# Kernel optimization log

Hardware: AMD Instinct MI355X
Metric: run time of the kernel (lower is better)

The kernel has to match this reference:

```python
import jax, jax.numpy as jnp
import numpy as np

D = 128
NQ = 25  # r2d2 quantized AP: 25 triangular bins over similarity range [0, 1]


def grid_sample_bilinear(img, grid):
    """F.grid_sample, mode='bilinear', padding_mode='zeros', align_corners=False.
    img: (B,C,H,W), grid: (B,Hg,Wg,2) in [-1,1] (x, y order). -> (B,C,Hg,Wg)"""
    B, C, H, W = img.shape
    gx = ((grid[..., 0] + 1.0) * W - 1.0) * 0.5  # (B,Hg,Wg) unnormalized x
    gy = ((grid[..., 1] + 1.0) * H - 1.0) * 0.5
    x0f = jnp.floor(gx)
    y0f = jnp.floor(gy)
    wx1 = gx - x0f
    wy1 = gy - y0f
    x0 = x0f.astype(jnp.int32)
    y0 = y0f.astype(jnp.int32)

    def gather(yi, xi):
        valid = ((xi >= 0) & (xi < W) & (yi >= 0) & (yi < H)).astype(img.dtype)
        xc = jnp.clip(xi, 0, W - 1)
        yc = jnp.clip(yi, 0, H - 1)
        v = jax.vmap(lambda im, y, x: im[:, y, x])(img, yc, xc)  # (B,C,Hg,Wg)
        return v * valid[:, None]

    out = (gather(y0, x0) * ((1 - wy1) * (1 - wx1))[:, None]
           + gather(y0, x0 + 1) * ((1 - wy1) * wx1)[:, None]
           + gather(y0 + 1, x0) * (wy1 * (1 - wx1))[:, None]
           + gather(y0 + 1, x0 + 1) * (wy1 * wx1)[:, None])
    return out


def quantized_ap(sim, lab):
    """r2d2 QAPLoss: soft-histogram differentiable AP.
    sim: (B,N,M) similarities, lab: (B,N,M) binary labels (float). -> (B,N) AP per query."""
    a = jnp.float32(NQ - 1)                 # slope; bin width = 1/a over gap [0,1]
    c = jnp.linspace(1.0, 0.0, NQ, dtype=sim.dtype)  # bin centers, descending score
    # triangular kernel membership: relu(1 - a*|s - c|), shape (B,N,Q,M)
    q = jnp.maximum(0.0, 1.0 - a * jnp.abs(sim[:, :, None, :] - c[None, None, :, None]))
    nbs = q.sum(-1)                          # (B,N,Q) soft count per bin
    rec = (q * lab[:, :, None, :]).sum(-1)   # (B,N,Q) soft positive count per bin
    prec = jnp.cumsum(rec, -1) / (1e-16 + jnp.cumsum(nbs, -1))
    rec = rec / rec.sum(-1, keepdims=True)
    return (prec * rec).sum(-1)              # (B,N)


def setup_inputs() -> dict:
    key = jax.random.key(0)
    k1, k2, k3, k4, k5 = jax.random.split(key, 5)
    B, H, W = 2, 32, 32
    d1 = jax.random.normal(k1, (B, D, H, W), dtype=jnp.float32)
    d2 = jax.random.normal(k2, (B, D, H, W), dtype=jnp.float32)
    # L2-normalize over channels (r2d2 descriptors are unit-norm -> sims in [-1,1])
    d1 = d1 / jnp.linalg.norm(d1, axis=1, keepdims=True)
    d2 = d2 / jnp.linalg.norm(d2, axis=1, keepdims=True)
    rel = jax.random.uniform(k3, (B, 1, H, W), dtype=jnp.float32)
    grid = jax.random.uniform(k4, (B, H, W, 2), dtype=jnp.float32) * 1.8 - 0.9  # in [-0.9,0.9]
    label = jax.random.randint(k5, (B, H, W, H, W), 0, 2, dtype=jnp.int32)
    return {"desc1": d1, "desc2": d2, "reliability": rel, "grid": grid, "label": label}


def reference(desc1, desc2, reliability, grid, label):
    B, C, H, W = desc1.shape
    d2w = grid_sample_bilinear(desc2, grid)           # warp image2 descriptors
    q = desc1.reshape(B, C, H * W).transpose(0, 2, 1)  # (B,N,C)
    db = d2w.reshape(B, C, H * W).transpose(0, 2, 1)   # (B,M,C)
    sim = jnp.einsum('bnd,bmd->bnm', q, db)            # per-sample pairwise similarity
    lab = label.reshape(B, H * W, H * W).astype(sim.dtype)
    ap = quantized_ap(sim, lab)                        # (B,N)
    return jnp.mean(ap)                                # mAP over queries and batch
```

## Files before the change

### kernel.cpp

```cpp
#include <hip/hip_runtime.h>


#define NQB 25

template<int CTRL>
__device__ __forceinline__ float dppadd(float v) {
    int s = __builtin_amdgcn_update_dpp(0, __float_as_int(v), CTRL, 0xf, 0xf, true);
    return v + __int_as_float(s);
}
__device__ __forceinline__ float red16(float v) {
    v = dppadd<0xB1>(v);
    v = dppadd<0x4E>(v);
    v = dppadd<0x141>(v);
    v = dppadd<0x140>(v);
    return v;
}

__device__ __forceinline__ void loadc(const float* __restrict__ dp, int ch,
                                      float* d)
{
    int cb = ch << 3;
#pragma unroll
    for (int i = 0; i < 8; i++) {
        d[i]     = dp[(size_t)(cb + i) << 10];
        d[8 + i] = dp[(((size_t)(cb + i)) << 10) + 512];
    }
}
__device__ __forceinline__ void fmac(const float* __restrict__ d1, int ch,
                                     const float* d, float* a0, float* a1)
{
    int cb = ch << 3;
#pragma unroll
    for (int i = 0; i < 8; i++) {
        const float* qp = d1 + ((size_t)(cb + i) << 10);
#pragma unroll
        for (int qq = 0; qq < 8; qq++) {
            float qv = qp[qq];
            a0[qq] = fmaf(qv, d[i], a0[qq]);
            a1[qq] = fmaf(qv, d[8 + i], a1[qq]);
        }
    }
}

__global__ __launch_bounds__(512) void k_main(const float* __restrict__ desc1,
                                              const float* __restrict__ desc2,
                                              const float* __restrict__ grd,
                                              const int* __restrict__ label,
                                              float* __restrict__ appart)
{
    __shared__ float s[8][1024];
    __shared__ float CNs[8][4][NQB];
    __shared__ float CRs[8][4][NQB];
    __shared__ float apb[8];

    int tid = threadIdx.x;
    int qg0 = blockIdx.x << 3;
    int b = qg0 >> 10;
    int n0 = qg0 & 1023;

    int q = tid >> 6, l = tid & 63;
    const int* lp = label + ((size_t)(qg0 + q) << 10) + l;
    int lv[16];
#pragma unroll
    for (int e = 0; e < 16; e++) lv[e] = lp[(size_t)(e << 6)];
    const float2* gp = (const float2*)grd + ((size_t)b << 10) + l;
    float2 gv[16];
#pragma unroll
    for (int e = 0; e < 16; e++) gv[e] = gp[(size_t)(e << 6)];

    const float* d1 = desc1 + ((size_t)b << 17) + n0;
    const float* dp = desc2 + ((size_t)b << 17) + tid;

    float a0[8], a1[8];
#pragma unroll
    for (int qq = 0; qq < 8; qq++) { a0[qq] = 0.f; a1[qq] = 0.f; }

    float dA[16], dB[16];
    loadc(dp, 0, dA);
    for (int ch = 0; ch < 16; ch += 2) {
        loadc(dp, ch + 1, dB);
        fmac(d1, ch, dA, a0, a1);
        if (ch + 2 < 16) loadc(dp, ch + 2, dA);
        fmac(d1, ch + 1, dB, a0, a1);
    }
#pragma unroll
    for (int qq = 0; qq < 8; qq++) { s[qq][tid] = a0[qq]; s[qq][tid + 512] = a1[qq]; }
    __syncthreads();

    float CN[NQB], CR[NQB];
#pragma unroll
    for (int k = 0; k < NQB; k++) { CN[k] = 0.f; CR[k] = 0.f; }
    const float* sq = s[q];
#pragma unroll
    for (int e = 0; e < 16; e++) {
        float gx = gv[e].x, gy = gv[e].y;
        float fx = ((gx + 1.f) * 32.f - 1.f) * 0.5f;
        float fy = ((gy + 1.f) * 32.f - 1.f) * 0.5f;
        float x0f = floorf(fx), y0f = floorf(fy);
        float wx1 = fx - x0f, wy1 = fy - y0f;
        float wx0 = 1.f - wx1, wy0 = 1.f - wy1;
        int x0 = (int)x0f, y0 = (int)y0f;
        int x1 = x0 + 1, y1 = y0 + 1;
        bool bx0 = (unsigned)x0 < 32u, bx1 = (unsigned)x1 < 32u;
        bool by0 = (unsigned)y0 < 32u, by1 = (unsigned)y1 < 32u;
        float w00 = (by0 && bx0) ? wy0 * wx0 : 0.f;
        float w01 = (by0 && bx1) ? wy0 * wx1 : 0.f;
        float w10 = (by1 && bx0) ? wy1 * wx0 : 0.f;
        float w11 = (by1 && bx1) ? wy1 * wx1 : 0.f;
        int xc0 = min(max(x0, 0), 31), xc1 = min(max(x1, 0), 31);
        int yc0 = min(max(y0, 0), 31), yc1 = min(max(y1, 0), 31);
        float sv = w00 * sq[(yc0 << 5) + xc0];
        sv = fmaf(w01, sq[(yc0 << 5) + xc1], sv);
        sv = fmaf(w10, sq[(yc1 << 5) + xc0], sv);
        sv = fmaf(w11, sq[(yc1 << 5) + xc1], sv);

        float u = fmaf(-24.f, sv, 24.f);
        float lfv = (float)lv[e];
#pragma unroll
        for (int k = 0; k < NQB; k++) {
            float t = fminf(fmaxf((float)(k + 1) - u, 0.f), 1.f);
            CN[k] += t;
            CR[k] = fmaf(lfv, t, CR[k]);
        }
    }
#pragma unroll
    for (int k = 0; k < NQB; k++) { CN[k] = red16(CN[k]); CR[k] = red16(CR[k]); }
    if ((l & 15) == 0) {
        int rec = l >> 4;
#pragma unroll
        for (int k = 0; k < NQB; k++) { CNs[q][rec][k] = CN[k]; CRs[q][rec][k] = CR[k]; }
    }
    __syncthreads();

    if (tid < 8) {
        float ap = 0.f, prev = 0.f;
#pragma unroll
        for (int k = 0; k < NQB; k++) {
            float cn = CNs[tid][0][k] + CNs[tid][1][k] + CNs[tid][2][k] + CNs[tid][3][k];
            float cr = CRs[tid][0][k] + CRs[tid][1][k] + CRs[tid][2][k] + CRs[tid][3][k];
            float pr = cr / (1e-16f + cn);
            ap += pr * (cr - prev);
            prev = cr;
        }
        apb[tid] = ap / prev;
    }
    __syncthreads();
    if (tid == 0) {
        float v = 0.f;
#pragma unroll
        for (int q2 = 0; q2 < 8; q2++) v += apb[q2];
        appart[blockIdx.x] = v;
    }
}

__global__ __launch_bounds__(256) void k_final(const float* __restrict__ appart,
                                               float* __restrict__ out,
                                               int nb, float invn)
{
    int tid = threadIdx.x;
    float v = 0.f;
    for (int i = tid; i < nb; i += 256) v += appart[i];
    for (int off = 32; off; off >>= 1) v += __shfl_xor(v, off, 64);
    __shared__ float wsum[4];
    if ((tid & 63) == 0) wsum[tid >> 6] = v;
    __syncthreads();
    if (tid == 0) out[0] = (wsum[0] + wsum[1] + wsum[2] + wsum[3]) * invn;
}

extern "C" void kernel_launch(void* const* d_in, const int* in_sizes, int n_in,
                              void* d_out, int out_size, void* d_ws, size_t ws_size,
                              hipStream_t stream)
{
    const float* desc1 = (const float*)d_in[0];
    const float* desc2 = (const float*)d_in[1];
    const float* grd   = (const float*)d_in[3];
    const int*   label = (const int*)d_in[4];

    int B = in_sizes[0] / (128 * 1024);
    int npos = B * 1024;
    int nblk = npos / 8;

    float* ws = (float*)d_ws;
    float* appart = ws;
    float* out = (float*)d_out;

    k_main<<<nblk, 512, 0, stream>>>(desc1, desc2, grd, label, appart);
    k_final<<<1, 256, 0, stream>>>(appart, out, nblk, 1.f / (float)npos);
}
```

Measured before the change: 25.63 us.

## Replace per-bin clamp accumulation with shared-memory sparse histogram scatter

Each element now touches only the two triangular bins it overlaps, instead of evaluating all 25 cumulative clamp terms. It does this with LDS atomic adds into a per-thread column of a large shared histogram, covering both counts and positives. A column reduction over the histogram and a prefix sum in the AP loop then rebuild the cumulative counts, replacing the DPP reductions. The cost is about 106KB of extra LDS that must be zeroed and read back, plus 64 LDS atomics per thread. This cuts occupancy and adds memory traffic in exchange for far fewer VALU ops.

```diff
diff --git a/kernel.cpp b/kernel.cpp
--- a/kernel.cpp
+++ b/kernel.cpp
@@ -2,19 +2,6 @@
 
 
 #define NQB 25
-
-template<int CTRL>
-__device__ __forceinline__ float dppadd(float v) {
-    int s = __builtin_amdgcn_update_dpp(0, __float_as_int(v), CTRL, 0xf, 0xf, true);
-    return v + __int_as_float(s);
-}
-__device__ __forceinline__ float red16(float v) {
-    v = dppadd<0xB1>(v);
-    v = dppadd<0x4E>(v);
-    v = dppadd<0x141>(v);
-    v = dppadd<0x140>(v);
-    return v;
-}
 
 __device__ __forceinline__ void loadc(const float* __restrict__ dp, int ch,
                                       float* d)
@@ -49,14 +36,21 @@
                                               float* __restrict__ appart)
 {
     __shared__ float s[8][1024];
-    __shared__ float CNs[8][4][NQB];
-    __shared__ float CRs[8][4][NQB];
+    __shared__ float H[52][512];
+    __shared__ float Eb[8][52];
     __shared__ float apb[8];
 
     int tid = threadIdx.x;
     int qg0 = blockIdx.x << 3;
     int b = qg0 >> 10;
     int n0 = qg0 & 1023;
+
+    {
+        float4 z4; z4.x = 0.f; z4.y = 0.f; z4.z = 0.f; z4.w = 0.f;
+        float4* hz = (float4*)&H[0][0];
+#pragma unroll
+        for (int i = 0; i < 13; i++) hz[(i << 9) + tid] = z4;
+    }
 
     int q = tid >> 6, l = tid & 63;
     const int* lp = label + ((size_t)(qg0 + q) << 10) + l;
@@ -87,10 +81,8 @@
     for (int qq = 0; qq < 8; qq++) { s[qq][tid] = a0[qq]; s[qq][tid + 512] = a1[qq]; }
     __syncthreads();
 
-    float CN[NQB], CR[NQB];
-#pragma unroll
-    for (int k = 0; k < NQB; k++) { CN[k] = 0.f; CR[k] = 0.f; }
     const float* sq = s[q];
+    float* Hc = &H[0][tid];
 #pragma unroll
     for (int e = 0; e < 16; e++) {
         float gx = gv[e].x, gy = gv[e].y;
@@ -114,30 +106,40 @@
         sv = fmaf(w10, sq[(yc1 << 5) + xc0], sv);
         sv = fmaf(w11, sq[(yc1 << 5) + xc1], sv);
 
-        float u = fmaf(-24.f, sv, 24.f);
-        float lfv = (float)lv[e];
-#pragma unroll
-        for (int k = 0; k < NQB; k++) {
-            float t = fminf(fmaxf((float)(k + 1) - u, 0.f), 1.f);
-            CN[k] += t;
-            CR[k] = fmaf(lfv, t, CR[k]);
+        float u = fmaxf(fmaf(-24.f, sv, 24.f), 0.f);
+        int ku = (int)u;
+        float frac = (float)(ku + 1) - u;
+        if (ku <= 24) {
+            atomicAdd(&Hc[(size_t)(ku << 9)], frac);
+            if (lv[e]) atomicAdd(&Hc[(size_t)((26 + ku) << 9)], frac);
+        }
+        if (ku <= 23) {
+            float g = 1.f - frac;
+            atomicAdd(&Hc[(size_t)((ku + 1) << 9)], g);
+            if (lv[e]) atomicAdd(&Hc[(size_t)((27 + ku) << 9)], g);
         }
     }
+    __syncthreads();
+
+    if (tid < 416) {
+        int q2 = tid / 52, j = tid - q2 * 52;
+        const float4* row = (const float4*)&H[j][q2 << 6];
+        float ssum = 0.f;
 #pragma unroll
-    for (int k = 0; k < NQB; k++) { CN[k] = red16(CN[k]); CR[k] = red16(CR[k]); }
-    if ((l & 15) == 0) {
-        int rec = l >> 4;
-#pragma unroll
-        for (int k = 0; k < NQB; k++) { CNs[q][rec][k] = CN[k]; CRs[q][rec][k] = CR[k]; }
+        for (int i = 0; i < 16; i++) {
+            float4 v4 = row[i];
+            ssum += v4.x + v4.y + v4.z + v4.w;
+        }
+        Eb[q2][j] = ssum;
     }
     __syncthreads();
 
     if (tid < 8) {
-        float ap = 0.f, prev = 0.f;
+        float ap = 0.f, prev = 0.f, cn = 0.f, cr = 0.f;
 #pragma unroll
         for (int k = 0; k < NQB; k++) {
-            float cn = CNs[tid][0][k] + CNs[tid][1][k] + CNs[tid][2][k] + CNs[tid][3][k];
-            float cr = CRs[tid][0][k] + CRs[tid][1][k] + CRs[tid][2][k] + CRs[tid][3][k];
+            cn += Eb[tid][k];
+            cr += Eb[tid][26 + k];
             float pr = cr / (1e-16f + cn);
             ap += pr * (cr - prev);
             prev = cr;
```

New measurement: 43.39 us. 69.3% more time.
